# Kernel optimization log

Measured on AMD Instinct MI355X. Metric: run time of the kernel, lower is better.

The kernel has to match this reference:

```python
import jax, jax.numpy as jnp
import numpy as np

H, SK, SV, PK, PV = 8, 16, 16, 4, 8
EPS = 1e-8
NUM_LOGITS = 3
SCALE_SCALAR = (NUM_LOGITS * SK) ** -0.5
SCALE_POINT = (NUM_LOGITS * PK * (9.0 / 2.0)) ** -0.5
SCALE_PAIR = NUM_LOGITS ** -0.5


def setup_inputs() -> dict:
    key = jax.random.key(0)
    ks = jax.random.split(key, 16)
    b, n, dim, pdim = 1, 512, 384, 128
    s = 0.02
    return {
        "single_repr": jax.random.normal(ks[0], (b, n, dim), jnp.float32),
        "pairwise_repr": jax.random.normal(ks[1], (b, n, n, pdim), jnp.float32),
        "rotations": jax.random.normal(ks[2], (b, n, 3, 3), jnp.float32),
        "translations": jax.random.normal(ks[3], (b, n, 3), jnp.float32),
        "Wsq": jax.random.normal(ks[4], (dim, H * SK), jnp.float32) * s,
        "Wsk": jax.random.normal(ks[5], (dim, H * SK), jnp.float32) * s,
        "Wsv": jax.random.normal(ks[6], (dim, H * SV), jnp.float32) * s,
        "Wpq": jax.random.normal(ks[7], (dim, H * PK * 3), jnp.float32) * s,
        "Wpk": jax.random.normal(ks[8], (dim, H * PK * 3), jnp.float32) * s,
        "Wpv": jax.random.normal(ks[9], (dim, H * PV * 3), jnp.float32) * s,
        "point_weights": jnp.log(jnp.exp(jnp.ones((H,), jnp.float32)) - 1.0),
        "Wpair": jax.random.normal(ks[10], (pdim, H), jnp.float32) * s,
        "bpair": jnp.zeros((H,), jnp.float32),
        "Wout": jax.random.normal(ks[11], (H * (SV + pdim + PV * 4), dim), jnp.float32) * s,
        "bout": jnp.zeros((dim,), jnp.float32),
    }


def reference(single_repr, pairwise_repr, rotations, translations,
              Wsq, Wsk, Wsv, Wpq, Wpk, Wpv, point_weights, Wpair, bpair, Wout, bout):
    x = single_repr
    b, n, _ = x.shape

    # scalar q/k/v: [b, n, h, d]
    q_s = (x @ Wsq).reshape(b, n, H, SK)
    k_s = (x @ Wsk).reshape(b, n, H, SK)
    v_s = (x @ Wsv).reshape(b, n, H, SV)

    # point q/k/v in local frame: [b, n, h, d, 3], then rotate + translate to global frame
    def to_global(t, d):
        p = t.reshape(b, n, H, d, 3)
        return jnp.einsum('bnhdc,bncr->bnhdr', p, rotations) + translations[:, :, None, None, :]

    q_p = to_global(x @ Wpq, PK)   # [b,n,h,pk,3]
    k_p = to_global(x @ Wpk, PK)
    v_p = to_global(x @ Wpv, PV)   # [b,n,h,pv,3]

    # scalar logits [b,h,i,j]
    logits_scalar = jnp.einsum('bihd,bjhd->bhij', q_s, k_s) * SCALE_SCALAR

    # point-distance logits: sum over (d,c) of (q_i - k_j)^2
    q_ph = jnp.transpose(q_p, (0, 2, 1, 3, 4))  # [b,h,i,pk,3]
    k_ph = jnp.transpose(k_p, (0, 2, 1, 3, 4))
    diff = q_ph[:, :, :, None] - k_ph[:, :, None]          # [b,h,i,j,pk,3]
    dist2 = jnp.sum(diff * diff, axis=(-2, -1))            # [b,h,i,j]
    pw = jax.nn.softplus(point_weights)[None, :, None, None]
    logits_points = -0.5 * pw * SCALE_POINT * dist2

    # pairwise bias logits
    logits_pair = jnp.transpose(pairwise_repr @ Wpair + bpair, (0, 3, 1, 2)) * SCALE_PAIR

    attn = jax.nn.softmax(logits_scalar + logits_points + logits_pair, axis=-1)  # [b,h,i,j]

    # scalar output
    res_scalar = jnp.einsum('bhij,bjhd->bihd', attn, v_s).reshape(b, n, H * SV)

    # pairwise output
    res_pair = jnp.einsum('bhij,bijd->bihd', attn, pairwise_repr).reshape(b, n, -1)

    # point output: attend, then map back to local frame with R^T
    v_ph = jnp.transpose(v_p, (0, 2, 1, 3, 4))             # [b,h,j,pv,3]
    res_p = jnp.einsum('bhij,bhjdc->bhidc', attn, v_ph)    # [b,h,i,pv,3] (global)
    res_p = res_p - translations[:, None, :, None, :]
    res_p = jnp.einsum('bhndc,bnrc->bhndr', res_p, rotations)  # R^T applied
    res_p_norm = jnp.sqrt(jnp.sum(res_p * res_p, axis=-1) + EPS)  # [b,h,n,pv]
    res_p = jnp.transpose(res_p, (0, 2, 1, 3, 4)).reshape(b, n, H * PV * 3)
    res_p_norm = jnp.transpose(res_p_norm, (0, 2, 1, 3)).reshape(b, n, H * PV)

    results = jnp.concatenate([res_scalar, res_p, res_p_norm, res_pair], axis=-1)
    return results @ Wout + bout
```

## Files before the change

kernel.cpp:

```cpp
#include <hip/hip_runtime.h>
#include <math.h>

#define NTOK 512
#define DIM 384
#define PDIM 128
#define H 8

#define QKB_STRIDE 224
#define VB_STRIDE  320
#define RES_STRIDE 1408
#define PART_STRIDE 1360
#define KS 4
#define KC (RES_STRIDE / KS)

static constexpr float SCALE_SCALAR = 0.14433756729740643f;
static constexpr float SCALE_POINT  = 0.13608276348795434f;
static constexpr float SCALE_PAIR   = 0.57735026918962580f;

__global__ __launch_bounds__(192) void ipa_proj(
    const float* __restrict__ x, const float* __restrict__ rot, const float* __restrict__ trans,
    const float* __restrict__ Wsq, const float* __restrict__ Wsk, const float* __restrict__ Wsv,
    const float* __restrict__ Wpq, const float* __restrict__ Wpk, const float* __restrict__ Wpv,
    float* __restrict__ qB, float* __restrict__ kB, float* __restrict__ vB)
{
  const int tt = blockIdx.x, cg = blockIdx.y, tid = threadIdx.x;
  __shared__ float s_x[4][DIM];
  __shared__ float s_p[4][192];
  __shared__ float s_R[4][9];
  __shared__ float s_T[4][3];

  {
    const float4* xg = reinterpret_cast<const float4*>(x + (size_t)(tt * 4) * DIM);
    float4* sx4 = reinterpret_cast<float4*>(&s_x[0][0]);
    sx4[tid] = xg[tid];
    sx4[tid + 192] = xg[tid + 192];
  }
  if (tid < 36) s_R[tid / 9][tid % 9] = rot[(size_t)(tt * 4) * 9 + tid];
  if (tid >= 64 && tid < 76) s_T[(tid - 64) / 3][(tid - 64) % 3] = trans[(size_t)(tt * 4) * 3 + (tid - 64)];
  __syncthreads();

  const int c = cg * 192 + tid;
  const float* W; int ncols, lc;
  if      (c < 128) { W = Wsq; ncols = 128; lc = c; }
  else if (c < 256) { W = Wsk; ncols = 128; lc = c - 128; }
  else if (c < 384) { W = Wsv; ncols = 128; lc = c - 256; }
  else if (c < 480) { W = Wpq; ncols = 96;  lc = c - 384; }
  else if (c < 576) { W = Wpk; ncols = 96;  lc = c - 480; }
  else              { W = Wpv; ncols = 192; lc = c - 576; }

  float acc[4] = {};
  const float* wp = W + lc;
#pragma unroll 8
  for (int k = 0; k < DIM; ++k) {
    float w = *wp; wp += ncols;
#pragma unroll
    for (int tok = 0; tok < 4; ++tok) acc[tok] += w * s_x[tok][k];
  }

  if (cg < 2) {
#pragma unroll
    for (int tok = 0; tok < 4; ++tok) {
      const int i = tt * 4 + tok;
      if (c < 128)      qB[(size_t)i * QKB_STRIDE + c] = acc[tok];
      else if (c < 256) kB[(size_t)i * QKB_STRIDE + (c - 128)] = acc[tok];
      else              vB[(size_t)i * VB_STRIDE + (c - 256)] = acc[tok];
    }
  } else {
#pragma unroll
    for (int tok = 0; tok < 4; ++tok) s_p[tok][tid] = acc[tok];
    __syncthreads();
    for (int t = tid; t < 256; t += 192) {
      const int tok = t >> 6, tr = t & 63;
      const int i = tt * 4 + tok;
      const float* R = s_R[tok];
      const float* T = s_T[tok];
      const float* src; float* dst;
      if (cg == 2) {
        if (tr < 32) { src = &s_p[tok][tr * 3];             dst = qB + (size_t)i * QKB_STRIDE + 128 + tr * 3; }
        else         { src = &s_p[tok][96 + (tr - 32) * 3]; dst = kB + (size_t)i * QKB_STRIDE + 128 + (tr - 32) * 3; }
      } else {
        src = &s_p[tok][tr * 3]; dst = vB + (size_t)i * VB_STRIDE + 128 + tr * 3;
      }
      float px = src[0], py = src[1], pz = src[2];
#pragma unroll
      for (int r = 0; r < 3; ++r)
        dst[r] = px * R[0 * 3 + r] + py * R[1 * 3 + r] + pz * R[2 * 3 + r] + T[r];
    }
  }
}

__global__ __launch_bounds__(256) void ipa_attn_part(
    const float* __restrict__ pair, const float* __restrict__ pw,
    const float* __restrict__ Wpair, const float* __restrict__ bpair,
    const float* __restrict__ qB, const float* __restrict__ kB,
    const float* __restrict__ vB, float* __restrict__ partial,
    int NC, int JR, int NT)
{
  const int c = blockIdx.x, i = blockIdx.y, tid = threadIdx.x;

  __shared__ float4 s_pT4[2048];
  __shared__ float  s_wpT[H][PDIM];
  __shared__ float  s_e[4][2][64];
  __shared__ float  s_qs[128];
  __shared__ float  s_qp[96];
  __shared__ float  s_coef[H], s_bp[H];

  for (int t = tid; t < PDIM * H; t += 256) {
    const int h = t >> 7, d = t & 127;
    s_wpT[h][d] = Wpair[d * 8 + h] * SCALE_PAIR;
  }
  if (tid < 224) {
    float v = qB[(size_t)i * QKB_STRIDE + tid];
    if (tid < 128) s_qs[tid] = v; else s_qp[tid - 128] = v;
  }
  if (tid < H) {
    s_coef[tid] = -0.5f * log1pf(__expf(pw[tid])) * SCALE_POINT;
    s_bp[tid]   = bpair[tid] * SCALE_PAIR;
  }

  const int hp = tid >> 6, jl = tid & 63;
  const int h0 = 2 * hp, h1 = h0 + 1;
  const int h = tid >> 5, u = tid & 31;
  const int ovb0 = (u < 16) ? (h * 16 + u) : (128 + h * 24 + (u - 16));
  const int ovb1 = 128 + h * 24 + 16 + u;

  float m0 = -1e30f, m1 = -1e30f, l0 = 0.f, l1 = 0.f;
  float4 accp = make_float4(0.f, 0.f, 0.f, 0.f);
  float accv0 = 0.f, accv1 = 0.f;

  for (int t = 0; t < NT; ++t) {
    float4 r[8];
    {
      const float4* g = reinterpret_cast<const float4*>(
          pair + ((size_t)i * NTOK + (size_t)c * JR + (size_t)t * 64) * PDIM);
#pragma unroll
      for (int k = 0; k < 8; ++k) r[k] = g[tid + 256 * k];
    }
    __syncthreads();
#pragma unroll
    for (int k = 0; k < 8; ++k) {
      const int f = tid + 256 * k;
      s_pT4[(f & 31) * 64 + ((f >> 5) ^ (f & 7))] = r[k];
    }
    __syncthreads();

    float4 pa0v = make_float4(0.f, 0.f, 0.f, 0.f), pa1v = pa0v;
    {
      const float4* w0p = reinterpret_cast<const float4*>(&s_wpT[h0][0]);
      const float4* w1p = reinterpret_cast<const float4*>(&s_wpT[h1][0]);
#pragma unroll 8
      for (int d4 = 0; d4 < 32; ++d4) {
        float4 p = s_pT4[d4 * 64 + (jl ^ (d4 & 7))];
        float4 w0 = w0p[d4], w1 = w1p[d4];
        pa0v.x += p.x * w0.x; pa0v.y += p.y * w0.y; pa0v.z += p.z * w0.z; pa0v.w += p.w * w0.w;
        pa1v.x += p.x * w1.x; pa1v.y += p.y * w1.y; pa1v.z += p.z * w1.z; pa1v.w += p.w * w1.w;
      }
    }
    const float pa0 = pa0v.x + pa0v.y + pa0v.z + pa0v.w;
    const float pa1 = pa1v.x + pa1v.y + pa1v.z + pa1v.w;

    const int j = c * JR + t * 64 + jl;
    const float4* kr4 = reinterpret_cast<const float4*>(kB + (size_t)j * QKB_STRIDE);
    float sa0 = 0.f, sa1 = 0.f;
    {
      const float4* qs4 = reinterpret_cast<const float4*>(s_qs);
#pragma unroll
      for (int tq = 0; tq < 4; ++tq) {
        float4 q = qs4[h0 * 4 + tq], k = kr4[h0 * 4 + tq];
        sa0 += q.x * k.x + q.y * k.y + q.z * k.z + q.w * k.w;
        float4 q2 = qs4[h1 * 4 + tq], k2 = kr4[h1 * 4 + tq];
        sa1 += q2.x * k2.x + q2.y * k2.y + q2.z * k2.z + q2.w * k2.w;
      }
    }
    float da0 = 0.f, da1 = 0.f;
    {
      const float4* qp4 = reinterpret_cast<const float4*>(s_qp);
#pragma unroll
      for (int tq = 0; tq < 3; ++tq) {
        float4 q = qp4[h0 * 3 + tq], k = kr4[32 + h0 * 3 + tq];
        float d0 = q.x - k.x, d1 = q.y - k.y, d2 = q.z - k.z, d3 = q.w - k.w;
        da0 += d0 * d0 + d1 * d1 + d2 * d2 + d3 * d3;
        float4 q2 = qp4[h1 * 3 + tq], k2 = kr4[32 + h1 * 3 + tq];
        float e0d = q2.x - k2.x, e1d = q2.y - k2.y, e2d = q2.z - k2.z, e3d = q2.w - k2.w;
        da1 += e0d * e0d + e1d * e1d + e2d * e2d + e3d * e3d;
      }
    }
    float lg0 = sa0 * SCALE_SCALAR + s_coef[h0] * da0 + pa0 + s_bp[h0];
    float lg1 = sa1 * SCALE_SCALAR + s_coef[h1] * da1 + pa1 + s_bp[h1];

    float tm0 = lg0, tm1 = lg1;
#pragma unroll
    for (int off = 32; off; off >>= 1) {
      tm0 = fmaxf(tm0, __shfl_xor(tm0, off, 64));
      tm1 = fmaxf(tm1, __shfl_xor(tm1, off, 64));
    }
    const float m0n = fmaxf(m0, tm0), m1n = fmaxf(m1, tm1);
    const float sc0 = __expf(m0 - m0n), sc1 = __expf(m1 - m1n);
    const float e0 = __expf(lg0 - m0n), e1 = __expf(lg1 - m1n);
    float ts0 = e0, ts1 = e1;
#pragma unroll
    for (int off = 32; off; off >>= 1) {
      ts0 += __shfl_xor(ts0, off, 64);
      ts1 += __shfl_xor(ts1, off, 64);
    }
    m0 = m0n; m1 = m1n;
    l0 = l0 * sc0 + ts0;
    l1 = l1 * sc1 + ts1;
    s_e[hp][0][jl] = e0;
    s_e[hp][1][jl] = e1;

    const float sc = (tid & 32) ? sc1 : sc0;
    accp.x *= sc; accp.y *= sc; accp.z *= sc; accp.w *= sc;
    accv0 *= sc; accv1 *= sc;
    const float* erow = &s_e[hp][(tid >> 5) & 1][0];
    const float* vrow = vB + (size_t)(c * JR + t * 64) * VB_STRIDE;
#pragma unroll 8
    for (int j2 = 0; j2 < 64; ++j2) {
      const float e = erow[j2];
      float4 p = s_pT4[u * 64 + (j2 ^ (u & 7))];
      accp.x += e * p.x; accp.y += e * p.y; accp.z += e * p.z; accp.w += e * p.w;
      accv0 += e * vrow[ovb0];
      if (u < 8) accv1 += e * vrow[ovb1];
      vrow += VB_STRIDE;
    }
  }

  float* part = partial + ((size_t)i * NC + c) * PART_STRIDE;
  if ((tid & 63) == 0) {
    part[h0] = m0; part[h1] = m1;
    part[8 + h0] = l0; part[8 + h1] = l1;
  }
  *reinterpret_cast<float4*>(part + 336 + h * 128 + u * 4) = accp;
  if (u < 16) part[16 + h * 16 + u] = accv0;
  else        part[144 + h * 24 + (u - 16)] = accv0;
  if (u < 8)  part[144 + h * 24 + 16 + u] = accv1;
}

__global__ __launch_bounds__(256) void ipa_combine(
    const float* __restrict__ partial, const float* __restrict__ rot,
    const float* __restrict__ trans, float* __restrict__ results, int NC)
{
  const int i = blockIdx.x, tid = threadIdx.x;
  __shared__ float s_f[8][H];
  __shared__ float s_invL[H];
  __shared__ float s_res[RES_STRIDE];
  __shared__ float s_pt[192];
  __shared__ float s_R[9], s_T[3];

  const float* pb = partial + (size_t)i * NC * PART_STRIDE;
  if (tid < H) {
    float M = -1e30f;
    for (int cc = 0; cc < NC; ++cc) M = fmaxf(M, pb[cc * PART_STRIDE + tid]);
    float L = 0.f;
    for (int cc = 0; cc < NC; ++cc) {
      float f = __expf(pb[cc * PART_STRIDE + tid] - M);
      s_f[cc][tid] = f;
      L += f * pb[cc * PART_STRIDE + 8 + tid];
    }
    s_invL[tid] = 1.f / L;
  }
  if (tid >= 32 && tid < 41) s_R[tid - 32] = rot[i * 9 + (tid - 32)];
  if (tid >= 48 && tid < 51) s_T[tid - 48] = trans[i * 3 + (tid - 48)];
  __syncthreads();

  for (int idx = tid; idx < 1344; idx += 256) {
    int hh, ofs;
    if (idx < 128)      { hh = idx >> 4;          ofs = 16 + idx; }
    else if (idx < 320) { hh = (idx - 128) / 24;  ofs = 144 + (idx - 128); }
    else                { hh = (idx - 320) >> 7;  ofs = 336 + (idx - 320); }
    float v = 0.f;
    for (int cc = 0; cc < NC; ++cc) v += s_f[cc][hh] * pb[cc * PART_STRIDE + ofs];
    v *= s_invL[hh];
    if (idx < 128)      s_res[idx] = v;
    else if (idx < 320) s_pt[idx - 128] = v;
    else                s_res[384 + (idx - 320)] = v;
  }
  __syncthreads();

  if (tid < 64) {
    const int hh = tid >> 3, p = tid & 7;
    const int base = hh * 24 + p * 3;
    float gx = s_pt[base]     - s_T[0];
    float gy = s_pt[base + 1] - s_T[1];
    float gz = s_pt[base + 2] - s_T[2];
    float lx = gx * s_R[0] + gy * s_R[1] + gz * s_R[2];
    float ly = gx * s_R[3] + gy * s_R[4] + gz * s_R[5];
    float lz = gx * s_R[6] + gy * s_R[7] + gz * s_R[8];
    s_res[128 + base]     = lx;
    s_res[128 + base + 1] = ly;
    s_res[128 + base + 2] = lz;
    s_res[320 + hh * 8 + p] = sqrtf(lx * lx + ly * ly + lz * lz + 1e-8f);
  }
  __syncthreads();

  float4* dst = reinterpret_cast<float4*>(results + (size_t)i * RES_STRIDE);
  const float4* src = reinterpret_cast<const float4*>(s_res);
  for (int t = tid; t < RES_STRIDE / 4; t += 256) dst[t] = src[t];
}

__global__ __launch_bounds__(256) void ipa_out1(
    const float* __restrict__ results, const float* __restrict__ Wout,
    float* __restrict__ pout)
{
  const int tt = blockIdx.x, ct = blockIdx.y, ks = blockIdx.z, tid = threadIdx.x;
  __shared__ float s_a[32][40];
  __shared__ float s_w[32][64];
  const int tx = tid & 15, ty = tid >> 4;
  float acc[2][4] = {};

  for (int kc = 0; kc < KC / 32; ++kc) {
    const int k0 = ks * KC + kc * 32;
    __syncthreads();
    {
      const int tok = tid >> 3, kq = tid & 7;
      *reinterpret_cast<float4*>(&s_a[tok][kq * 4]) =
          *reinterpret_cast<const float4*>(results + (size_t)(tt * 32 + tok) * RES_STRIDE + k0 + kq * 4);
    }
#pragma unroll
    for (int rr = 0; rr < 2; ++rr) {
      const int tq = tid + rr * 256;
      const int kk = tq >> 4, c4 = tq & 15;
      *reinterpret_cast<float4*>(&s_w[kk][c4 * 4]) =
          *reinterpret_cast<const float4*>(Wout + (size_t)(k0 + kk) * DIM + ct * 64 + c4 * 4);
    }
    __syncthreads();
#pragma unroll 8
    for (int kk = 0; kk < 32; ++kk) {
      const float a0 = s_a[ty][kk], a1 = s_a[ty + 16][kk];
#pragma unroll
      for (int cc = 0; cc < 4; ++cc) {
        const float w = s_w[kk][tx + 16 * cc];
        acc[0][cc] += a0 * w;
        acc[1][cc] += a1 * w;
      }
    }
  }
#pragma unroll
  for (int rr = 0; rr < 2; ++rr)
#pragma unroll
    for (int cc = 0; cc < 4; ++cc)
      pout[((size_t)ks * NTOK + tt * 32 + ty + 16 * rr) * DIM + ct * 64 + tx + 16 * cc] = acc[rr][cc];
}

__global__ __launch_bounds__(256) void ipa_out2(
    const float* __restrict__ pout, const float* __restrict__ bout, float* __restrict__ out)
{
  const int idx = blockIdx.x * 256 + threadIdx.x;
  const float4* p4 = reinterpret_cast<const float4*>(pout);
  float4 v = p4[idx];
#pragma unroll
  for (int ks = 1; ks < KS; ++ks) {
    float4 w = p4[idx + ks * (NTOK * DIM / 4)];
    v.x += w.x; v.y += w.y; v.z += w.z; v.w += w.w;
  }
  const float4 b = reinterpret_cast<const float4*>(bout)[idx % (DIM / 4)];
  v.x += b.x; v.y += b.y; v.z += b.z; v.w += b.w;
  reinterpret_cast<float4*>(out)[idx] = v;
}

extern "C" void kernel_launch(void* const* d_in, const int* in_sizes, int n_in,
                              void* d_out, int out_size, void* d_ws, size_t ws_size,
                              hipStream_t stream) {
  const float* x     = (const float*)d_in[0];
  const float* pair  = (const float*)d_in[1];
  const float* rot   = (const float*)d_in[2];
  const float* trans = (const float*)d_in[3];
  const float* Wsq   = (const float*)d_in[4];
  const float* Wsk   = (const float*)d_in[5];
  const float* Wsv   = (const float*)d_in[6];
  const float* Wpq   = (const float*)d_in[7];
  const float* Wpk   = (const float*)d_in[8];
  const float* Wpv   = (const float*)d_in[9];
  const float* pw    = (const float*)d_in[10];
  const float* Wpair = (const float*)d_in[11];
  const float* bpair = (const float*)d_in[12];
  const float* Wout  = (const float*)d_in[13];
  const float* bout  = (const float*)d_in[14];
  float* out = (float*)d_out;

  float* ws = (float*)d_ws;
  float* qB = ws;
  float* kB = qB + (size_t)NTOK * QKB_STRIDE;
  float* vB = kB + (size_t)NTOK * QKB_STRIDE;
  float* results = vB + (size_t)NTOK * VB_STRIDE;
  float* partial = results + (size_t)NTOK * RES_STRIDE;
  float* pout = partial;

  const size_t base_f = (size_t)NTOK * QKB_STRIDE * 2 + (size_t)NTOK * VB_STRIDE
                      + (size_t)NTOK * RES_STRIDE;
  const size_t pout_f = (size_t)KS * NTOK * DIM;
  int NC = 8;
  while (NC > 1) {
    size_t region = (size_t)NTOK * NC * PART_STRIDE;
    if (region < pout_f) region = pout_f;
    if ((base_f + region) * 4 <= ws_size) break;
    NC >>= 1;
  }
  const int JR = NTOK / NC;
  const int NT = JR / 64;

  ipa_proj<<<dim3(NTOK / 4, 4), 192, 0, stream>>>(x, rot, trans, Wsq, Wsk, Wsv, Wpq, Wpk, Wpv, qB, kB, vB);
  ipa_attn_part<<<dim3(NC, NTOK), 256, 0, stream>>>(pair, pw, Wpair, bpair, qB, kB, vB, partial, NC, JR, NT);
  ipa_combine<<<NTOK, 256, 0, stream>>>(partial, rot, trans, results, NC);
  ipa_out1<<<dim3(NTOK / 32, DIM / 64, KS), 256, 0, stream>>>(results, Wout, pout);
  ipa_out2<<<NTOK * DIM / 4 / 256, 256, 0, stream>>>(pout, bout, out);
}
```

Before: 511.6 us.

## Restructure attention partial kernel with direct global-to-LDS pair loads and fixed split

Hardcodes an 8-way key split so each attention block handles exactly one 64-key tile, dropping the online-softmax rescaling loop. The pair tile is loaded straight into LDS with the global_load_lds builtin in natural layout, and the bias dot product uses an XOR-swizzled read. The value accumulation moves to a separate 80-thread float4 pass. The output GEMM uses 8 K-splits with 16-wide K chunks. This removes the workspace-size fallback, so a smaller workspace could overflow, and the global_load_lds call with a 16-byte size may not be supported on every target.

```diff
diff --git a/kernel.cpp b/kernel.cpp
--- a/kernel.cpp
+++ b/kernel.cpp
@@ -5,12 +5,13 @@
 #define DIM 384
 #define PDIM 128
 #define H 8
+#define NC 8
 
 #define QKB_STRIDE 224
 #define VB_STRIDE  320
 #define RES_STRIDE 1408
 #define PART_STRIDE 1360
-#define KS 4
+#define KS 8
 #define KC (RES_STRIDE / KS)
 
 static constexpr float SCALE_SCALAR = 0.14433756729740643f;
@@ -93,155 +94,140 @@
     const float* __restrict__ pair, const float* __restrict__ pw,
     const float* __restrict__ Wpair, const float* __restrict__ bpair,
     const float* __restrict__ qB, const float* __restrict__ kB,
-    const float* __restrict__ vB, float* __restrict__ partial,
-    int NC, int JR, int NT)
+    const float* __restrict__ vB, float* __restrict__ partial)
 {
   const int c = blockIdx.x, i = blockIdx.y, tid = threadIdx.x;
 
   __shared__ float4 s_pT4[2048];
   __shared__ float  s_wpT[H][PDIM];
-  __shared__ float  s_e[4][2][64];
-  __shared__ float  s_qs[128];
-  __shared__ float  s_qp[96];
+  __shared__ float  s_e[H][65];
+  __shared__ float  s_lm[16];
   __shared__ float  s_coef[H], s_bp[H];
 
+  const int wv = tid >> 6, ln = tid & 63;
+  const int h0 = 2 * wv, h1 = h0 + 1;
+
+  const float4* kbase = reinterpret_cast<const float4*>(kB + (size_t)(c * 64 + ln) * QKB_STRIDE);
+  const float4* qbase = reinterpret_cast<const float4*>(qB + (size_t)i * QKB_STRIDE);
+  float sa0 = 0.f, sa1 = 0.f, da0 = 0.f, da1 = 0.f;
+#pragma unroll
+  for (int t = 0; t < 4; ++t) {
+    float4 q = qbase[h0 * 4 + t], k = kbase[h0 * 4 + t];
+    sa0 += q.x * k.x + q.y * k.y + q.z * k.z + q.w * k.w;
+    float4 q2 = qbase[h1 * 4 + t], k2 = kbase[h1 * 4 + t];
+    sa1 += q2.x * k2.x + q2.y * k2.y + q2.z * k2.z + q2.w * k2.w;
+  }
+#pragma unroll
+  for (int t = 0; t < 3; ++t) {
+    float4 q = qbase[32 + h0 * 3 + t], k = kbase[32 + h0 * 3 + t];
+    float d0 = q.x - k.x, d1 = q.y - k.y, d2 = q.z - k.z, d3 = q.w - k.w;
+    da0 += d0 * d0 + d1 * d1 + d2 * d2 + d3 * d3;
+    float4 q2 = qbase[32 + h1 * 3 + t], k2 = kbase[32 + h1 * 3 + t];
+    float e0 = q2.x - k2.x, e1 = q2.y - k2.y, e2 = q2.z - k2.z, e3 = q2.w - k2.w;
+    da1 += e0 * e0 + e1 * e1 + e2 * e2 + e3 * e3;
+  }
+
+  const float4* gsrc = reinterpret_cast<const float4*>(pair + ((size_t)i * NTOK + (size_t)c * 64) * PDIM);
+#if defined(__has_builtin) && __has_builtin(__builtin_amdgcn_global_load_lds)
+#pragma unroll
+  for (int w = 0; w < 8; ++w) {
+    __builtin_amdgcn_global_load_lds(
+        (const __attribute__((address_space(1))) float4*)(gsrc + ((wv * 8 + w) * 64 + ln)),
+        (__attribute__((address_space(3))) float4*)(&s_pT4[(wv * 8 + w) * 64]), 16, 0, 0);
+  }
+#else
+#pragma unroll
+  for (int w = 0; w < 8; ++w) {
+    const int s = (wv * 8 + w) * 64 + ln;
+    s_pT4[s] = gsrc[s];
+  }
+#endif
+
   for (int t = tid; t < PDIM * H; t += 256) {
-    const int h = t >> 7, d = t & 127;
-    s_wpT[h][d] = Wpair[d * 8 + h] * SCALE_PAIR;
-  }
-  if (tid < 224) {
-    float v = qB[(size_t)i * QKB_STRIDE + tid];
-    if (tid < 128) s_qs[tid] = v; else s_qp[tid - 128] = v;
+    const int d = t >> 3, h = t & 7;
+    s_wpT[h][d] = Wpair[t] * SCALE_PAIR;
   }
   if (tid < H) {
     s_coef[tid] = -0.5f * log1pf(__expf(pw[tid])) * SCALE_POINT;
     s_bp[tid]   = bpair[tid] * SCALE_PAIR;
   }
-
-  const int hp = tid >> 6, jl = tid & 63;
-  const int h0 = 2 * hp, h1 = h0 + 1;
-  const int h = tid >> 5, u = tid & 31;
-  const int ovb0 = (u < 16) ? (h * 16 + u) : (128 + h * 24 + (u - 16));
-  const int ovb1 = 128 + h * 24 + 16 + u;
-
-  float m0 = -1e30f, m1 = -1e30f, l0 = 0.f, l1 = 0.f;
-  float4 accp = make_float4(0.f, 0.f, 0.f, 0.f);
-  float accv0 = 0.f, accv1 = 0.f;
-
-  for (int t = 0; t < NT; ++t) {
-    float4 r[8];
-    {
-      const float4* g = reinterpret_cast<const float4*>(
-          pair + ((size_t)i * NTOK + (size_t)c * JR + (size_t)t * 64) * PDIM);
-#pragma unroll
-      for (int k = 0; k < 8; ++k) r[k] = g[tid + 256 * k];
-    }
-    __syncthreads();
-#pragma unroll
-    for (int k = 0; k < 8; ++k) {
-      const int f = tid + 256 * k;
-      s_pT4[(f & 31) * 64 + ((f >> 5) ^ (f & 7))] = r[k];
-    }
-    __syncthreads();
-
-    float4 pa0v = make_float4(0.f, 0.f, 0.f, 0.f), pa1v = pa0v;
-    {
-      const float4* w0p = reinterpret_cast<const float4*>(&s_wpT[h0][0]);
-      const float4* w1p = reinterpret_cast<const float4*>(&s_wpT[h1][0]);
+  __syncthreads();
+
+  float pa0 = 0.f, pa1 = 0.f;
+  {
+    const int xo = ln & 7;
+    const float4* w0p = reinterpret_cast<const float4*>(&s_wpT[h0][0]);
+    const float4* w1p = reinterpret_cast<const float4*>(&s_wpT[h1][0]);
 #pragma unroll 8
-      for (int d4 = 0; d4 < 32; ++d4) {
-        float4 p = s_pT4[d4 * 64 + (jl ^ (d4 & 7))];
-        float4 w0 = w0p[d4], w1 = w1p[d4];
-        pa0v.x += p.x * w0.x; pa0v.y += p.y * w0.y; pa0v.z += p.z * w0.z; pa0v.w += p.w * w0.w;
-        pa1v.x += p.x * w1.x; pa1v.y += p.y * w1.y; pa1v.z += p.z * w1.z; pa1v.w += p.w * w1.w;
-      }
-    }
-    const float pa0 = pa0v.x + pa0v.y + pa0v.z + pa0v.w;
-    const float pa1 = pa1v.x + pa1v.y + pa1v.z + pa1v.w;
-
-    const int j = c * JR + t * 64 + jl;
-    const float4* kr4 = reinterpret_cast<const float4*>(kB + (size_t)j * QKB_STRIDE);
-    float sa0 = 0.f, sa1 = 0.f;
-    {
-      const float4* qs4 = reinterpret_cast<const float4*>(s_qs);
-#pragma unroll
-      for (int tq = 0; tq < 4; ++tq) {
-        float4 q = qs4[h0 * 4 + tq], k = kr4[h0 * 4 + tq];
-        sa0 += q.x * k.x + q.y * k.y + q.z * k.z + q.w * k.w;
-        float4 q2 = qs4[h1 * 4 + tq], k2 = kr4[h1 * 4 + tq];
-        sa1 += q2.x * k2.x + q2.y * k2.y + q2.z * k2.z + q2.w * k2.w;
-      }
-    }
-    float da0 = 0.f, da1 = 0.f;
-    {
-      const float4* qp4 = reinterpret_cast<const float4*>(s_qp);
-#pragma unroll
-      for (int tq = 0; tq < 3; ++tq) {
-        float4 q = qp4[h0 * 3 + tq], k = kr4[32 + h0 * 3 + tq];
-        float d0 = q.x - k.x, d1 = q.y - k.y, d2 = q.z - k.z, d3 = q.w - k.w;
-        da0 += d0 * d0 + d1 * d1 + d2 * d2 + d3 * d3;
-        float4 q2 = qp4[h1 * 3 + tq], k2 = kr4[32 + h1 * 3 + tq];
-        float e0d = q2.x - k2.x, e1d = q2.y - k2.y, e2d = q2.z - k2.z, e3d = q2.w - k2.w;
-        da1 += e0d * e0d + e1d * e1d + e2d * e2d + e3d * e3d;
-      }
-    }
-    float lg0 = sa0 * SCALE_SCALAR + s_coef[h0] * da0 + pa0 + s_bp[h0];
-    float lg1 = sa1 * SCALE_SCALAR + s_coef[h1] * da1 + pa1 + s_bp[h1];
-
-    float tm0 = lg0, tm1 = lg1;
-#pragma unroll
-    for (int off = 32; off; off >>= 1) {
-      tm0 = fmaxf(tm0, __shfl_xor(tm0, off, 64));
-      tm1 = fmaxf(tm1, __shfl_xor(tm1, off, 64));
-    }
-    const float m0n = fmaxf(m0, tm0), m1n = fmaxf(m1, tm1);
-    const float sc0 = __expf(m0 - m0n), sc1 = __expf(m1 - m1n);
-    const float e0 = __expf(lg0 - m0n), e1 = __expf(lg1 - m1n);
-    float ts0 = e0, ts1 = e1;
-#pragma unroll
-    for (int off = 32; off; off >>= 1) {
-      ts0 += __shfl_xor(ts0, off, 64);
-      ts1 += __shfl_xor(ts1, off, 64);
-    }
-    m0 = m0n; m1 = m1n;
-    l0 = l0 * sc0 + ts0;
-    l1 = l1 * sc1 + ts1;
-    s_e[hp][0][jl] = e0;
-    s_e[hp][1][jl] = e1;
-
-    const float sc = (tid & 32) ? sc1 : sc0;
-    accp.x *= sc; accp.y *= sc; accp.z *= sc; accp.w *= sc;
-    accv0 *= sc; accv1 *= sc;
-    const float* erow = &s_e[hp][(tid >> 5) & 1][0];
-    const float* vrow = vB + (size_t)(c * JR + t * 64) * VB_STRIDE;
+    for (int t = 0; t < 32; ++t) {
+      const int d4 = t ^ xo;
+      float4 p = s_pT4[ln * 32 + d4];
+      float4 w0 = w0p[d4], w1 = w1p[d4];
+      pa0 += p.x * w0.x + p.y * w0.y + p.z * w0.z + p.w * w0.w;
+      pa1 += p.x * w1.x + p.y * w1.y + p.z * w1.z + p.w * w1.w;
+    }
+  }
+  float lg0 = sa0 * SCALE_SCALAR + s_coef[h0] * da0 + pa0 + s_bp[h0];
+  float lg1 = sa1 * SCALE_SCALAR + s_coef[h1] * da1 + pa1 + s_bp[h1];
+
+  float m0 = lg0, m1 = lg1;
+#pragma unroll
+  for (int off = 32; off; off >>= 1) {
+    m0 = fmaxf(m0, __shfl_xor(m0, off, 64));
+    m1 = fmaxf(m1, __shfl_xor(m1, off, 64));
+  }
+  const float e0 = __expf(lg0 - m0), e1 = __expf(lg1 - m1);
+  float l0 = e0, l1 = e1;
+#pragma unroll
+  for (int off = 32; off; off >>= 1) {
+    l0 += __shfl_xor(l0, off, 64);
+    l1 += __shfl_xor(l1, off, 64);
+  }
+  s_e[h0][ln] = e0;
+  s_e[h1][ln] = e1;
+  if (ln == 0) {
+    s_lm[h0] = m0; s_lm[h1] = m1;
+    s_lm[8 + h0] = l0; s_lm[8 + h1] = l1;
+  }
+  __syncthreads();
+
+  float* part = partial + ((size_t)i * NC + c) * PART_STRIDE;
+
+  {
+    const int h = tid >> 5, u = tid & 31;
+    float4 accp = make_float4(0.f, 0.f, 0.f, 0.f);
 #pragma unroll 8
     for (int j2 = 0; j2 < 64; ++j2) {
-      const float e = erow[j2];
-      float4 p = s_pT4[u * 64 + (j2 ^ (u & 7))];
+      const float e = s_e[h][j2];
+      float4 p = s_pT4[j2 * 32 + u];
       accp.x += e * p.x; accp.y += e * p.y; accp.z += e * p.z; accp.w += e * p.w;
-      accv0 += e * vrow[ovb0];
-      if (u < 8) accv1 += e * vrow[ovb1];
-      vrow += VB_STRIDE;
-    }
-  }
-
-  float* part = partial + ((size_t)i * NC + c) * PART_STRIDE;
-  if ((tid & 63) == 0) {
-    part[h0] = m0; part[h1] = m1;
-    part[8 + h0] = l0; part[8 + h1] = l1;
-  }
-  *reinterpret_cast<float4*>(part + 336 + h * 128 + u * 4) = accp;
-  if (u < 16) part[16 + h * 16 + u] = accv0;
-  else        part[144 + h * 24 + (u - 16)] = accv0;
-  if (u < 8)  part[144 + h * 24 + 16 + u] = accv1;
+    }
+    *reinterpret_cast<float4*>(part + 336 + h * 128 + u * 4) = accp;
+  }
+
+  if (tid < 80) {
+    const int col4 = tid;
+    const int hv = (col4 < 32) ? (col4 >> 2) : (col4 - 32) / 6;
+    const float4* vb4 = reinterpret_cast<const float4*>(vB) + (size_t)(c * 64) * 80 + col4;
+    float4 accv = make_float4(0.f, 0.f, 0.f, 0.f);
+#pragma unroll 8
+    for (int j2 = 0; j2 < 64; ++j2) {
+      const float e = s_e[hv][j2];
+      float4 v = vb4[(size_t)j2 * 80];
+      accv.x += e * v.x; accv.y += e * v.y; accv.z += e * v.z; accv.w += e * v.w;
+    }
+    *reinterpret_cast<float4*>(part + 16 + col4 * 4) = accv;
+  }
+
+  if (tid < 16) part[tid] = s_lm[tid];
 }
 
 __global__ __launch_bounds__(256) void ipa_combine(
     const float* __restrict__ partial, const float* __restrict__ rot,
-    const float* __restrict__ trans, float* __restrict__ results, int NC)
+    const float* __restrict__ trans, float* __restrict__ results)
 {
   const int i = blockIdx.x, tid = threadIdx.x;
-  __shared__ float s_f[8][H];
+  __shared__ float s_f[NC][H];
   __shared__ float s_invL[H];
   __shared__ float s_res[RES_STRIDE];
   __shared__ float s_pt[192];
@@ -269,6 +255,7 @@
     else if (idx < 320) { hh = (idx - 128) / 24;  ofs = 144 + (idx - 128); }
     else                { hh = (idx - 320) >> 7;  ofs = 336 + (idx - 320); }
     float v = 0.f;
+#pragma unroll
     for (int cc = 0; cc < NC; ++cc) v += s_f[cc][hh] * pb[cc * PART_STRIDE + ofs];
     v *= s_invL[hh];
     if (idx < 128)      s_res[idx] = v;
@@ -303,29 +290,27 @@
     float* __restrict__ pout)
 {
   const int tt = blockIdx.x, ct = blockIdx.y, ks = blockIdx.z, tid = threadIdx.x;
-  __shared__ float s_a[32][40];
-  __shared__ float s_w[32][64];
+  __shared__ float s_a[32][20];
+  __shared__ float s_w[16][64];
   const int tx = tid & 15, ty = tid >> 4;
   float acc[2][4] = {};
 
-  for (int kc = 0; kc < KC / 32; ++kc) {
-    const int k0 = ks * KC + kc * 32;
+  for (int kc = 0; kc < 11; ++kc) {
+    const int k0 = ks * KC + kc * 16;
     __syncthreads();
+    if (tid < 128) {
+      const int row = tid >> 2, kq = tid & 3;
+      *reinterpret_cast<float4*>(&s_a[row][kq * 4]) =
+          *reinterpret_cast<const float4*>(results + (size_t)(tt * 32 + row) * RES_STRIDE + k0 + kq * 4);
+    }
     {
-      const int tok = tid >> 3, kq = tid & 7;
-      *reinterpret_cast<float4*>(&s_a[tok][kq * 4]) =
-          *reinterpret_cast<const float4*>(results + (size_t)(tt * 32 + tok) * RES_STRIDE + k0 + kq * 4);
-    }
-#pragma unroll
-    for (int rr = 0; rr < 2; ++rr) {
-      const int tq = tid + rr * 256;
-      const int kk = tq >> 4, c4 = tq & 15;
+      const int kk = tid >> 4, c4 = tid & 15;
       *reinterpret_cast<float4*>(&s_w[kk][c4 * 4]) =
           *reinterpret_cast<const float4*>(Wout + (size_t)(k0 + kk) * DIM + ct * 64 + c4 * 4);
     }
     __syncthreads();
-#pragma unroll 8
-    for (int kk = 0; kk < 32; ++kk) {
+#pragma unroll
+    for (int kk = 0; kk < 16; ++kk) {
       const float a0 = s_a[ty][kk], a1 = s_a[ty + 16][kk];
 #pragma unroll
       for (int cc = 0; cc < 4; ++cc) {
@@ -386,22 +371,9 @@
   float* partial = results + (size_t)NTOK * RES_STRIDE;
   float* pout = partial;
 
-  const size_t base_f = (size_t)NTOK * QKB_STRIDE * 2 + (size_t)NTOK * VB_STRIDE
-                      + (size_t)NTOK * RES_STRIDE;
-  const size_t pout_f = (size_t)KS * NTOK * DIM;
-  int NC = 8;
-  while (NC > 1) {
-    size_t region = (size_t)NTOK * NC * PART_STRIDE;
-    if (region < pout_f) region = pout_f;
-    if ((base_f + region) * 4 <= ws_size) break;
-    NC >>= 1;
-  }
-  const int JR = NTOK / NC;
-  const int NT = JR / 64;
-
   ipa_proj<<<dim3(NTOK / 4, 4), 192, 0, stream>>>(x, rot, trans, Wsq, Wsk, Wsv, Wpq, Wpk, Wpv, qB, kB, vB);
-  ipa_attn_part<<<dim3(NC, NTOK), 256, 0, stream>>>(pair, pw, Wpair, bpair, qB, kB, vB, partial, NC, JR, NT);
-  ipa_combine<<<NTOK, 256, 0, stream>>>(partial, rot, trans, results, NC);
+  ipa_attn_part<<<dim3(NC, NTOK), 256, 0, stream>>>(pair, pw, Wpair, bpair, qB, kB, vB, partial);
+  ipa_combine<<<NTOK, 256, 0, stream>>>(partial, rot, trans, results);
   ipa_out1<<<dim3(NTOK / 32, DIM / 64, KS), 256, 0, stream>>>(results, Wout, pout);
   ipa_out2<<<NTOK * DIM / 4 / 256, 256, 0, stream>>>(pout, bout, out);
 }
```

Measured after the change: 430.6 us. 1.19x faster.
